# Performance work log

Hardware: AMD Instinct MI355X
Metric: run time of the kernel (lower is better)

The kernel has to match this reference:

```python
import jax, jax.numpy as jnp
import numpy as np

BAND_LOW_MAX = 500.0
BAND_MID_MAX = 2000.0
ENERGY_THRESHOLD = 0.5

V, NH, NM = 1024, 16384, 16384


def setup_inputs() -> dict:
    key = jax.random.key(0)
    k1, k2, k3, k4, k5, k6 = jax.random.split(key, 6)
    harm_amps = jax.random.uniform(k1, (V, NH), dtype=jnp.float32)
    noise_mags = jax.random.uniform(k2, (V, NM), dtype=jnp.float32)
    # fundamental in [50, 1000) Hz so low/mid/high bands are all populated
    f0_hz = 50.0 + 950.0 * jax.random.uniform(k3, (V,), dtype=jnp.float32)
    competition_weight = 0.1 + jax.random.uniform(k4, (V,), dtype=jnp.float32)
    withdrawal = jax.random.uniform(k5, (V, 3), dtype=jnp.float32)  # [low, mid, high]
    is_active = jax.random.randint(k6, (V,), 0, 2).astype(bool)
    return {
        'harm_amps': harm_amps,
        'noise_mags': noise_mags,
        'f0_hz': f0_hz,
        'competition_weight': competition_weight,
        'withdrawal': withdrawal,
        'is_active': is_active,
    }


def reference(harm_amps, noise_mags, f0_hz, competition_weight, withdrawal, is_active):
    dt = harm_amps.dtype
    nh = harm_amps.shape[-1]
    actf = is_active.astype(dt)                     # [V]
    n_active = jnp.sum(is_active)

    harmonics = jnp.arange(1, nh + 1, dtype=dt)     # [NH]
    freqs = f0_hz[:, None] * harmonics[None, :]     # [V, NH]
    # bands partition the harmonics: 0=low (<500), 1=mid [500,2000), 2=high (>=2000)
    band_idx = (freqs >= BAND_LOW_MAX).astype(jnp.int32) + (freqs >= BAND_MID_MAX).astype(jnp.int32)  # [V, NH]

    # per-voice per-band energy (inactive voices contribute 0, as in the torch code)
    energy = jnp.stack(
        [jnp.sum(jnp.where(band_idx == b, harm_amps, jnp.zeros((), dt)), axis=-1) for b in range(3)],
        axis=1,
    ) * actf[:, None]                               # [V, 3]

    total_energy = jnp.sum(energy, axis=0)          # [3]
    total_weight = jnp.sum(competition_weight * actf)

    claim_ratio = competition_weight / jnp.maximum(total_weight, 1e-6)  # [V]
    my_share = claim_ratio * ENERGY_THRESHOLD                           # [V]
    excess = energy - my_share[:, None]                                 # [V, 3]
    excess_ratio = excess / jnp.maximum(energy, 1e-6)                   # [V, 3]
    reduction = jnp.maximum(0.3, 1.0 - withdrawal * excess_ratio * 0.5) # [V, 3]

    # reduction only applies when band is crowded, voice has energy, and voice exceeds its share
    apply = (total_energy[None, :] > ENERGY_THRESHOLD) & (energy > 0.0) & (excess > 0.0) & is_active[:, None]
    gain = jnp.where(apply, reduction, jnp.ones((), dt))                # [V, 3]

    elem_gain = jnp.take_along_axis(gain, band_idx, axis=1)             # [V, NH]
    harm_new = harm_amps * elem_gain

    total_before = jnp.sum(harm_amps, axis=-1)      # [V]
    total_after = jnp.sum(harm_new, axis=-1)        # [V]
    noise_scale = jnp.where(total_before > 1e-6, total_after / total_before, jnp.ones((), dt))
    noise_new = noise_mags * jnp.where(is_active, noise_scale, jnp.ones((), dt))[:, None]

    # inactive voices pass through unchanged
    harm_new = jnp.where(is_active[:, None], harm_new, harm_amps)

    # fewer than 2 active voices -> no competition at all
    changed = n_active >= 2
    harm_out = jnp.where(changed, harm_new, harm_amps)
    noise_out = jnp.where(changed, noise_new, noise_mags)
    # concat harm and noise outputs along last axis: [V, NH + NM]
    return jnp.concatenate([harm_out, noise_out], axis=-1)
```

## Files before the change

kernel.cpp:

```cpp
#include <hip/hip_runtime.h>

#define V   1024
#define NH  16384
#define NM  16384

#define BAND_LOW_MAX    500.0f
#define BAND_MID_MAX    2000.0f
#define ENERGY_THRESHOLD 0.5f

typedef float f32x4 __attribute__((ext_vector_type(4)));

__global__ __launch_bounds__(256)
void k1_stats(const float* __restrict__ harm,
              const float* __restrict__ f0_hz,
              const float* __restrict__ cw,
              const int*   __restrict__ is_active,
              float* __restrict__ stats ) {
    const int v   = blockIdx.x;
    const int tid = threadIdx.x;
    const float f0 = f0_hz[v];
    const f32x4* hrow = (const f32x4*)harm + (size_t)v * 4096;

    float e0 = 0.f, e1 = 0.f, e2 = 0.f;
    #pragma unroll
    for (int k = 0; k < 16; ++k) {
        const f32x4 a = hrow[tid + k * 256];
        const int hbase = (tid + k * 256) * 4;
        #pragma unroll
        for (int j = 0; j < 4; ++j) {
            const float freq = f0 * (float)(hbase + j + 1);
            if (freq < BAND_LOW_MAX)       e0 += a[j];
            else if (freq < BAND_MID_MAX)  e1 += a[j];
            else                           e2 += a[j];
        }
    }
    for (int off = 32; off > 0; off >>= 1) {
        e0 += __shfl_down(e0, off);
        e1 += __shfl_down(e1, off);
        e2 += __shfl_down(e2, off);
    }
    __shared__ float s[3][4];
    const int wid  = tid >> 6;
    const int lane = tid & 63;
    if (lane == 0) { s[0][wid] = e0; s[1][wid] = e1; s[2][wid] = e2; }
    __syncthreads();
    if (tid == 0) {
        const float t0 = s[0][0] + s[0][1] + s[0][2] + s[0][3];
        const float t1 = s[1][0] + s[1][1] + s[1][2] + s[1][3];
        const float t2 = s[2][0] + s[2][1] + s[2][2] + s[2][3];
        const float af = (is_active[v] != 0) ? 1.0f : 0.0f;
        stats[0 * V + v] = t0 * af;
        stats[1 * V + v] = t1 * af;
        stats[2 * V + v] = t2 * af;
        stats[3 * V + v] = cw[v] * af;
        stats[4 * V + v] = af;
    }
}

__global__ __launch_bounds__(256)
void k2_apply(const float* __restrict__ harm,
              const float* __restrict__ noise,
              const float* __restrict__ f0_hz,
              const float* __restrict__ cw,
              const float* __restrict__ wd,
              const int*   __restrict__ is_active,
              const float* __restrict__ stats,
              float* __restrict__ out) {
    const int bid  = blockIdx.x;
    const int v    = bid >> 3;
    const int part = bid & 7;
    const int tid  = threadIdx.x;

    const f32x4* sp = (const f32x4*)stats;
    const f32x4 x0 = sp[0 * 256 + tid];
    const f32x4 x1 = sp[1 * 256 + tid];
    const f32x4 x2 = sp[2 * 256 + tid];
    const f32x4 x3 = sp[3 * 256 + tid];
    const f32x4 x4 = sp[4 * 256 + tid];
    float r0 = (x0[0] + x0[1]) + (x0[2] + x0[3]);
    float r1 = (x1[0] + x1[1]) + (x1[2] + x1[3]);
    float r2 = (x2[0] + x2[1]) + (x2[2] + x2[3]);
    float r3 = (x3[0] + x3[1]) + (x3[2] + x3[3]);
    float r4 = (x4[0] + x4[1]) + (x4[2] + x4[3]);
    for (int off = 32; off > 0; off >>= 1) {
        r0 += __shfl_down(r0, off);
        r1 += __shfl_down(r1, off);
        r2 += __shfl_down(r2, off);
        r3 += __shfl_down(r3, off);
        r4 += __shfl_down(r4, off);
    }
    __shared__ float s2[5][4];
    const int wid  = tid >> 6;
    const int lane = tid & 63;
    if (lane == 0) {
        s2[0][wid] = r0; s2[1][wid] = r1; s2[2][wid] = r2;
        s2[3][wid] = r3; s2[4][wid] = r4;
    }
    __syncthreads();
    const float TE[3] = {
        s2[0][0] + s2[0][1] + s2[0][2] + s2[0][3],
        s2[1][0] + s2[1][1] + s2[1][2] + s2[1][3],
        s2[2][0] + s2[2][1] + s2[2][2] + s2[2][3] };
    const float TW = s2[3][0] + s2[3][1] + s2[3][2] + s2[3][3];
    const float NA = s2[4][0] + s2[4][1] + s2[4][2] + s2[4][3];

    const bool  act     = (is_active[v] != 0);
    const bool  changed = (NA >= 1.5f);
    const float w       = cw[v];
    const float share   = (w / fmaxf(TW, 1e-6f)) * ENERGY_THRESHOLD;

    const float ea[3] = { stats[0 * V + v], stats[1 * V + v], stats[2 * V + v] };

    const float tbefore = ea[0] + ea[1] + ea[2];
    float tafter = 0.f;
    float g[3];
    #pragma unroll
    for (int b = 0; b < 3; ++b) {
        const float excess = ea[b] - share;
        const float exr    = excess / fmaxf(ea[b], 1e-6f);
        const float red    = fmaxf(0.3f, 1.0f - wd[v * 3 + b] * exr * 0.5f);
        const bool apply   = (TE[b] > ENERGY_THRESHOLD) && (ea[b] > 0.0f) &&
                             (excess > 0.0f) && act;
        const float gb = apply ? red : 1.0f;
        tafter += gb * ea[b];
        g[b] = changed ? gb : 1.0f;
    }
    const float nscale = (tbefore > 1e-6f) ? (tafter / tbefore) : 1.0f;
    const float nse    = (changed && act) ? nscale : 1.0f;
    const float g0 = g[0], g1 = g[1], g2 = g[2];

    f32x4* orow = (f32x4*)out + (size_t)v * 8192;
    if (part < 4) {
        const float f0 = f0_hz[v];
        const f32x4* hrow = (const f32x4*)harm + (size_t)v * 4096;
        const int c0 = part * 1024 + tid;
        #pragma unroll
        for (int k = 0; k < 4; ++k) {
            const int c = c0 + k * 256;
            const f32x4 a = hrow[c];
            f32x4 o;
            #pragma unroll
            for (int j = 0; j < 4; ++j) {
                const float freq = f0 * (float)(c * 4 + j + 1);
                const float gg = (freq < BAND_LOW_MAX) ? g0
                               : (freq < BAND_MID_MAX) ? g1 : g2;
                o[j] = a[j] * gg;
            }
            __builtin_nontemporal_store(o, orow + c);
        }
    } else {
        const f32x4* nrow = (const f32x4*)noise + (size_t)v * 4096;
        const int c0 = (part - 4) * 1024 + tid;
        #pragma unroll
        for (int k = 0; k < 4; ++k) {
            const int c = c0 + k * 256;
            const f32x4 n = nrow[c];
            __builtin_nontemporal_store(n * nse, orow + 4096 + c);
        }
    }
}

extern "C" void kernel_launch(void* const* d_in, const int* in_sizes, int n_in,
                              void* d_out, int out_size, void* d_ws, size_t ws_size,
                              hipStream_t stream) {
    const float* harm  = (const float*)d_in[0];
    const float* noise = (const float*)d_in[1];
    const float* f0    = (const float*)d_in[2];
    const float* cw    = (const float*)d_in[3];
    const float* wd    = (const float*)d_in[4];
    const int*   act   = (const int*)d_in[5];
    float* out   = (float*)d_out;
    float* stats = (float*)d_ws;

    k1_stats<<<V, 256, 0, stream>>>(harm, f0, cw, act, stats);
    k2_apply<<<V * 8, 256, 0, stream>>>(harm, noise, f0, cw, wd, act, stats, out);
}
```

Baseline: 56.89 us.

## Compute per-voice gains once in last k1 block instead of every k2 block

Adds a last-block-done atomic counter to the stats kernel so the final block reduces global totals and computes per-voice band gains and noise scale once, writing them to a small gains buffer. The apply kernel then reads a single float4 per voice instead of redoing the 1024-voice reduction in each of its 8192 blocks. The cost is an extra memset launch, a threadfence plus atomic per block, and a serialized tail block at the end of k1.

```diff
diff --git a/kernel.cpp b/kernel.cpp
--- a/kernel.cpp
+++ b/kernel.cpp
@@ -14,8 +14,11 @@
 void k1_stats(const float* __restrict__ harm,
               const float* __restrict__ f0_hz,
               const float* __restrict__ cw,
+              const float* __restrict__ wd,
               const int*   __restrict__ is_active,
-              float* __restrict__ stats ) {
+              float* __restrict__ stats ,
+              float* __restrict__ gains ,
+              unsigned int* __restrict__ counter) {
     const int v   = blockIdx.x;
     const int tid = threadIdx.x;
     const float f0 = f0_hz[v];
@@ -40,6 +43,7 @@
         e2 += __shfl_down(e2, off);
     }
     __shared__ float s[3][4];
+    __shared__ bool is_last;
     const int wid  = tid >> 6;
     const int lane = tid & 63;
     if (lane == 0) { s[0][wid] = e0; s[1][wid] = e1; s[2][wid] = e2; }
@@ -54,47 +58,35 @@
         stats[2 * V + v] = t2 * af;
         stats[3 * V + v] = cw[v] * af;
         stats[4 * V + v] = af;
+        __threadfence();
+        const unsigned int old = __hip_atomic_fetch_add(
+            counter, 1u, __ATOMIC_ACQ_REL, __HIP_MEMORY_SCOPE_AGENT);
+        is_last = (old == V - 1);
     }
-}
+    __syncthreads();
+    if (!is_last) return;
 
-__global__ __launch_bounds__(256)
-void k2_apply(const float* __restrict__ harm,
-              const float* __restrict__ noise,
-              const float* __restrict__ f0_hz,
-              const float* __restrict__ cw,
-              const float* __restrict__ wd,
-              const int*   __restrict__ is_active,
-              const float* __restrict__ stats,
-              float* __restrict__ out) {
-    const int bid  = blockIdx.x;
-    const int v    = bid >> 3;
-    const int part = bid & 7;
-    const int tid  = threadIdx.x;
-
-    const f32x4* sp = (const f32x4*)stats;
-    const f32x4 x0 = sp[0 * 256 + tid];
-    const f32x4 x1 = sp[1 * 256 + tid];
-    const f32x4 x2 = sp[2 * 256 + tid];
-    const f32x4 x3 = sp[3 * 256 + tid];
-    const f32x4 x4 = sp[4 * 256 + tid];
-    float r0 = (x0[0] + x0[1]) + (x0[2] + x0[3]);
-    float r1 = (x1[0] + x1[1]) + (x1[2] + x1[3]);
-    float r2 = (x2[0] + x2[1]) + (x2[2] + x2[3]);
-    float r3 = (x3[0] + x3[1]) + (x3[2] + x3[3]);
-    float r4 = (x4[0] + x4[1]) + (x4[2] + x4[3]);
-    for (int off = 32; off > 0; off >>= 1) {
-        r0 += __shfl_down(r0, off);
-        r1 += __shfl_down(r1, off);
-        r2 += __shfl_down(r2, off);
-        r3 += __shfl_down(r3, off);
-        r4 += __shfl_down(r4, off);
+    float sv[5][4];
+    #pragma unroll
+    for (int p = 0; p < 5; ++p) {
+        #pragma unroll
+        for (int j = 0; j < 4; ++j) {
+            sv[p][j] = __hip_atomic_load(&stats[p * V + 4 * tid + j],
+                                         __ATOMIC_RELAXED, __HIP_MEMORY_SCOPE_AGENT);
+        }
     }
+    float r[5];
+    #pragma unroll
+    for (int p = 0; p < 5; ++p)
+        r[p] = (sv[p][0] + sv[p][1]) + (sv[p][2] + sv[p][3]);
+    #pragma unroll
+    for (int p = 0; p < 5; ++p)
+        for (int off = 32; off > 0; off >>= 1)
+            r[p] += __shfl_down(r[p], off);
     __shared__ float s2[5][4];
-    const int wid  = tid >> 6;
-    const int lane = tid & 63;
     if (lane == 0) {
-        s2[0][wid] = r0; s2[1][wid] = r1; s2[2][wid] = r2;
-        s2[3][wid] = r3; s2[4][wid] = r4;
+        #pragma unroll
+        for (int p = 0; p < 5; ++p) s2[p][wid] = r[p];
     }
     __syncthreads();
     const float TE[3] = {
@@ -103,35 +95,56 @@
         s2[2][0] + s2[2][1] + s2[2][2] + s2[2][3] };
     const float TW = s2[3][0] + s2[3][1] + s2[3][2] + s2[3][3];
     const float NA = s2[4][0] + s2[4][1] + s2[4][2] + s2[4][3];
+    const bool changed = (NA >= 1.5f);
 
-    const bool  act     = (is_active[v] != 0);
-    const bool  changed = (NA >= 1.5f);
-    const float w       = cw[v];
-    const float share   = (w / fmaxf(TW, 1e-6f)) * ENERGY_THRESHOLD;
+    f32x4* g4 = (f32x4*)gains;
+    #pragma unroll
+    for (int j = 0; j < 4; ++j) {
+        const int vv = 4 * tid + j;
+        const bool  act   = (sv[4][j] > 0.5f);
+        const float w     = sv[3][j];
+        const float share = (w / fmaxf(TW, 1e-6f)) * ENERGY_THRESHOLD;
+        const float ea[3] = { sv[0][j], sv[1][j], sv[2][j] };
 
-    const float ea[3] = { stats[0 * V + v], stats[1 * V + v], stats[2 * V + v] };
+        const float tbefore = ea[0] + ea[1] + ea[2];
+        float tafter = 0.f;
+        float g[3];
+        #pragma unroll
+        for (int b = 0; b < 3; ++b) {
+            const float excess = ea[b] - share;
+            const float exr    = excess / fmaxf(ea[b], 1e-6f);
+            const float red    = fmaxf(0.3f, 1.0f - wd[vv * 3 + b] * exr * 0.5f);
+            const bool apply   = (TE[b] > ENERGY_THRESHOLD) && (ea[b] > 0.0f) &&
+                                 (excess > 0.0f) && act;
+            const float gb = apply ? red : 1.0f;
+            tafter += gb * ea[b];
+            g[b] = changed ? gb : 1.0f;
+        }
+        const float nscale = (tbefore > 1e-6f) ? (tafter / tbefore) : 1.0f;
+        f32x4 gv;
+        gv[0] = g[0]; gv[1] = g[1]; gv[2] = g[2];
+        gv[3] = (changed && act) ? nscale : 1.0f;
+        g4[vv] = gv;
+    }
+}
 
-    const float tbefore = ea[0] + ea[1] + ea[2];
-    float tafter = 0.f;
-    float g[3];
-    #pragma unroll
-    for (int b = 0; b < 3; ++b) {
-        const float excess = ea[b] - share;
-        const float exr    = excess / fmaxf(ea[b], 1e-6f);
-        const float red    = fmaxf(0.3f, 1.0f - wd[v * 3 + b] * exr * 0.5f);
-        const bool apply   = (TE[b] > ENERGY_THRESHOLD) && (ea[b] > 0.0f) &&
-                             (excess > 0.0f) && act;
-        const float gb = apply ? red : 1.0f;
-        tafter += gb * ea[b];
-        g[b] = changed ? gb : 1.0f;
-    }
-    const float nscale = (tbefore > 1e-6f) ? (tafter / tbefore) : 1.0f;
-    const float nse    = (changed && act) ? nscale : 1.0f;
-    const float g0 = g[0], g1 = g[1], g2 = g[2];
+__global__ __launch_bounds__(256)
+void k2_apply(const float* __restrict__ harm,
+              const float* __restrict__ noise,
+              const float* __restrict__ f0_hz,
+              const float* __restrict__ gains,
+              float* __restrict__ out) {
+    const int bid  = blockIdx.x;
+    const int v    = bid >> 3;
+    const int part = bid & 7;
+    const int tid  = threadIdx.x;
 
+    const f32x4 gv = ((const f32x4*)gains)[v];
     f32x4* orow = (f32x4*)out + (size_t)v * 8192;
+
     if (part < 4) {
         const float f0 = f0_hz[v];
+        const float g0 = gv[0], g1 = gv[1], g2 = gv[2];
         const f32x4* hrow = (const f32x4*)harm + (size_t)v * 4096;
         const int c0 = part * 1024 + tid;
         #pragma unroll
@@ -149,6 +162,7 @@
             __builtin_nontemporal_store(o, orow + c);
         }
     } else {
+        const float nse = gv[3];
         const f32x4* nrow = (const f32x4*)noise + (size_t)v * 4096;
         const int c0 = (part - 4) * 1024 + tid;
         #pragma unroll
@@ -169,9 +183,14 @@
     const float* cw    = (const float*)d_in[3];
     const float* wd    = (const float*)d_in[4];
     const int*   act   = (const int*)d_in[5];
-    float* out   = (float*)d_out;
+    float* out = (float*)d_out;
+
     float* stats = (float*)d_ws;
+    float* gains = stats + 5 * V;
+    unsigned int* counter = (unsigned int*)(gains + 4 * V);
 
-    k1_stats<<<V, 256, 0, stream>>>(harm, f0, cw, act, stats);
-    k2_apply<<<V * 8, 256, 0, stream>>>(harm, noise, f0, cw, wd, act, stats, out);
+    hipMemsetAsync(counter, 0, sizeof(unsigned int), stream);
+
+    k1_stats<<<V, 256, 0, stream>>>(harm, f0, cw, wd, act, stats, gains, counter);
+    k2_apply<<<V * 8, 256, 0, stream>>>(harm, noise, f0, gains, out);
 }
```

Result: slower. 100.2 us (+76.2%).
